# Performance work log

Measured on AMD Instinct MI355X. Metric: run time of the kernel, lower is better.

The kernel has to match this reference:

```python
import jax, jax.numpy as jnp
import numpy as np

B, C, N = 8, 512, 2048
C2 = C // 2
BN_EPS = 1e-5


def setup_inputs() -> dict:
    key = jax.random.key(0)
    ks = jax.random.split(key, 8)
    s = lambda fan_in: 1.0 / np.sqrt(fan_in)
    return {
        "q": jax.random.normal(ks[0], (B, C, N), jnp.float32),
        "x": jax.random.normal(ks[1], (B, C2, N), jnp.float32),
        "Wq": jax.random.normal(ks[2], (C2, C), jnp.float32) * s(C),
        "Wk": jax.random.normal(ks[3], (C2, C2), jnp.float32) * s(C2),
        "Wv": jax.random.normal(ks[4], (C2, C), jnp.float32) * s(C),
        "bv": jax.random.normal(ks[5], (C2,), jnp.float32) * 0.01,
        "Wt": jax.random.normal(ks[6], (C2, C2), jnp.float32) * s(C2),
        "bt": jax.random.normal(ks[7], (C2,), jnp.float32) * 0.01,
        "gamma": jnp.ones((C2,), jnp.float32),
        "beta": jnp.zeros((C2,), jnp.float32),
        "running_mean": jnp.zeros((C2,), jnp.float32),
        "running_var": jnp.ones((C2,), jnp.float32),
    }


def reference(q, x, Wq, Wk, Wv, bv, Wt, bt, gamma, beta, running_mean, running_var):
    # 1x1 convs are pointwise GEMMs over the channel dim
    x_q = jnp.einsum("oc,bcn->bno", Wq, q)                    # [B, N, C2]
    x_k = jnp.einsum("oc,bcn->bon", Wk, x)                    # [B, C2, N]
    x_v = jnp.einsum("oc,bcn->bon", Wv, q) + bv[None, :, None]  # [B, C2, N]
    energy = jnp.einsum("bnc,bcm->bnm", x_q, x_k)             # [B, N, N]
    attn = jax.nn.softmax(energy, axis=-1)
    # offset-attention L1 renormalization over the query axis (dim=1)
    attn = attn / (1e-9 + attn.sum(axis=1, keepdims=True))
    x_r = jnp.einsum("bcn,bnm->bcm", x_v, attn)               # [B, C2, N]
    h = jnp.einsum("oc,bcn->bon", Wt, x - x_r) + bt[None, :, None]
    # BatchNorm1d in eval mode with running statistics
    inv = gamma / jnp.sqrt(running_var + BN_EPS)
    h = h * inv[None, :, None] + (beta - running_mean * inv)[None, :, None]
    return jax.nn.relu(h) + x
```

## Files before the change

### kernel.cpp

```cpp
#include <hip/hip_runtime.h>
#include <cstdint>
#include <cstddef>

#define KB_  8
#define KC_  512
#define KC2_ 256
#define KN_  2048

typedef __attribute__((ext_vector_type(8))) __bf16 bf16x8;
typedef __attribute__((ext_vector_type(8))) unsigned short u16x8;
typedef __attribute__((ext_vector_type(4))) float f32x4;

__device__ __forceinline__ unsigned short f2bf(float f) {
  union { float f; unsigned u; } x; x.f = f;
  unsigned r = x.u + 0x7fffu + ((x.u >> 16) & 1u);
  return (unsigned short)(r >> 16);
}
__device__ __forceinline__ float bf2f(unsigned short h) {
  union { unsigned u; float f; } x; x.u = ((unsigned)h) << 16;
  return x.f;
}

#define GLD16(g, l) __builtin_amdgcn_global_load_lds( \
    (__attribute__((address_space(1))) void*)(g),     \
    (__attribute__((address_space(3))) void*)(l), 16, 0, 0)

#define WAIT_VM8()  asm volatile("s_waitcnt vmcnt(8)" ::: "memory")
#define WAIT_VM0()  asm volatile("s_waitcnt vmcnt(0)" ::: "memory")
#define BARRIER()   __builtin_amdgcn_s_barrier()

__device__ __forceinline__ void xcd_swizzle(int& bx, int& by, int& bz) {
  const int gx = gridDim.x, gy = gridDim.y;
  const int nb = gx * gy * (int)gridDim.z;
  int f = ((int)blockIdx.z * gy + (int)blockIdx.y) * gx + (int)blockIdx.x;
  if ((nb & 7) == 0) f = (f & 7) * (nb >> 3) + (f >> 3);
  const int gxy = gx * gy;
  bz = f / gxy; int rem = f - bz * gxy;
  by = rem / gx; bx = rem - by * gx;
}

__global__ __launch_bounds__(256) void cvt_kernel(const float* __restrict__ in,
                                                  unsigned short* __restrict__ out, int n) {
  int i = (blockIdx.x * 256 + threadIdx.x) * 4;
  if (i >= n) return;
  float4 f = *(const float4*)(in + i);
  ushort4 u = { f2bf(f.x), f2bf(f.y), f2bf(f.z), f2bf(f.w) };
  *(ushort4*)(out + i) = u;
}

__global__ __launch_bounds__(256) void cvt_pair_kernel(const float* __restrict__ in,
                                                       unsigned short* __restrict__ hi,
                                                       unsigned short* __restrict__ lo, int n) {
  int i = (blockIdx.x * 256 + threadIdx.x) * 4;
  if (i >= n) return;
  float4 f = *(const float4*)(in + i);
  ushort4 h = { f2bf(f.x), f2bf(f.y), f2bf(f.z), f2bf(f.w) };
  ushort4 l = { f2bf(f.x - bf2f(h.x)), f2bf(f.y - bf2f(h.y)),
                f2bf(f.z - bf2f(h.z)), f2bf(f.w - bf2f(h.w)) };
  *(ushort4*)(hi + i) = h;
  *(ushort4*)(lo + i) = l;
}

__global__ __launch_bounds__(256) void transpose_pair_kernel(const float* __restrict__ in,
                                                             long sIn,
                                                             unsigned short* __restrict__ hi,
                                                             unsigned short* __restrict__ lo,
                                                             long sOut, int R, int Cc) {
  int b = blockIdx.z;
  const float* I = in + (size_t)b * sIn;
  __shared__ float tile[64][65];
  int t = threadIdx.x;
  int r0 = blockIdx.y * 64, c0 = blockIdx.x * 64;
#pragma unroll
  for (int k = 0; k < 4; k++) {
    int vi = k * 256 + t, rr = vi >> 4, cv = vi & 15;
    float4 f = *(const float4*)&I[(size_t)(r0 + rr) * Cc + c0 + cv * 4];
    tile[rr][cv * 4 + 0] = f.x; tile[rr][cv * 4 + 1] = f.y;
    tile[rr][cv * 4 + 2] = f.z; tile[rr][cv * 4 + 3] = f.w;
  }
  __syncthreads();
#pragma unroll
  for (int k = 0; k < 4; k++) {
    int vi = k * 256 + t, cc = vi >> 4, rv = vi & 15;
    float f0 = tile[rv * 4 + 0][cc], f1 = tile[rv * 4 + 1][cc];
    float f2 = tile[rv * 4 + 2][cc], f3 = tile[rv * 4 + 3][cc];
    ushort4 h = { f2bf(f0), f2bf(f1), f2bf(f2), f2bf(f3) };
    ushort4 l = { f2bf(f0 - bf2f(h.x)), f2bf(f1 - bf2f(h.y)),
                  f2bf(f2 - bf2f(h.z)), f2bf(f3 - bf2f(h.w)) };
    size_t o = (size_t)b * sOut + (size_t)(c0 + cc) * R + r0 + rv * 4;
    *(ushort4*)&hi[o] = h;
    *(ushort4*)&lo[o] = l;
  }
}

__global__ __launch_bounds__(256) void rowreduce_kernel(const float* __restrict__ rowpart,
                                                        float* __restrict__ rsv) {
  int idx = blockIdx.x * 256 + threadIdx.x;
  const float* p = rowpart + (size_t)idx * 32;
  float s = 0.f;
#pragma unroll
  for (int k = 0; k < 32; k++) s += p[k];
  rsv[idx] = 1.0f / s;
}

__global__ __launch_bounds__(256) void denom_kernel(const unsigned short* __restrict__ uT,
                                                    const float* __restrict__ rsv,
                                                    float* __restrict__ denom) {
  int b = blockIdx.y;
  int m = blockIdx.x * 4 + (threadIdx.x >> 6);
  int lane = threadIdx.x & 63;
  const unsigned short* U = uT + ((size_t)b * KN_ + m) * KN_;
  const float* R = rsv + (size_t)b * KN_;
  float s = 0.f;
#pragma unroll
  for (int c = 0; c < 4; c++) {
    int n = c * 512 + lane * 8;
    u16x8 u = *(const u16x8*)&U[n];
    float4 r0 = *(const float4*)&R[n];
    float4 r1 = *(const float4*)&R[n + 4];
    s += bf2f(u[0]) * r0.x + bf2f(u[1]) * r0.y + bf2f(u[2]) * r0.z + bf2f(u[3]) * r0.w;
    s += bf2f(u[4]) * r1.x + bf2f(u[5]) * r1.y + bf2f(u[6]) * r1.z + bf2f(u[7]) * r1.w;
  }
#pragma unroll
  for (int o = 32; o > 0; o >>= 1) s += __shfl_xor(s, o, 64);
  if (lane == 0) denom[(size_t)b * KN_ + m] = s;
}

__global__ __launch_bounds__(256) void energy_kernel(
    const unsigned short* __restrict__ Ahi, const unsigned short* __restrict__ Alo,
    const unsigned short* __restrict__ Bhi, const unsigned short* __restrict__ Blo,
    unsigned short* __restrict__ uT, float* __restrict__ rowpart) {
  int bx, by, b;
  xcd_swizzle(bx, by, b);
  Ahi += (size_t)b * KN_ * KC2_; Alo += (size_t)b * KN_ * KC2_;
  Bhi += (size_t)b * KN_ * KC2_; Blo += (size_t)b * KN_ * KC2_;
  const int m0 = by * 128;
  const int n0 = bx * 128;
  __shared__ __align__(16) char smem[65536];
  const int t = threadIdx.x, lane = t & 63, w = t >> 6;
  const int wr = w >> 1, wc = w & 1;
  const int srow = t >> 2;
  const int scol = (((t & 3) ^ ((srow >> 1) & 3)) * 8);
  const int lr = lane & 15, lk = (lane >> 4) * 8;
  const int rsw = ((lr >> 1) & 3) << 4;

  auto STAGE = [&](char* dst, int kt) {
    const size_t ga = (size_t)(m0 + srow) * KC2_ + kt + scol;
    const size_t gb = (size_t)(n0 + srow) * KC2_ + kt + scol;
    GLD16(Ahi + ga, dst + 0 + w * 1024);
    GLD16(Ahi + ga + (size_t)64 * KC2_, dst + 4096 + w * 1024);
    GLD16(Alo + ga, dst + 8192 + w * 1024);
    GLD16(Alo + ga + (size_t)64 * KC2_, dst + 12288 + w * 1024);
    GLD16(Bhi + gb, dst + 16384 + w * 1024);
    GLD16(Bhi + gb + (size_t)64 * KC2_, dst + 20480 + w * 1024);
    GLD16(Blo + gb, dst + 24576 + w * 1024);
    GLD16(Blo + gb + (size_t)64 * KC2_, dst + 28672 + w * 1024);
  };

  f32x4 acc[4][4];
  const f32x4 z = {0.f, 0.f, 0.f, 0.f};
#pragma unroll
  for (int i = 0; i < 4; i++)
#pragma unroll
    for (int j = 0; j < 4; j++) acc[i][j] = z;

  STAGE(smem, 0);
  for (int kt8 = 0; kt8 < 8; kt8++) {
    char* cur = smem + (kt8 & 1) * 32768;
    char* nxt = smem + ((kt8 & 1) ^ 1) * 32768;
    if (kt8 < 7) {
      STAGE(nxt, (kt8 + 1) * 32);
      WAIT_VM8();
    } else {
      WAIT_VM0();
    }
    BARRIER();
    bf16x8 ah[4], al[4], bh[4], bl[4];
#pragma unroll
    for (int i = 0; i < 4; i++) {
      int ro = (wr * 64 + i * 16 + lr) * 64 + ((lk * 2) ^ rsw);
      ah[i] = *(const bf16x8*)(cur + 0 + ro);
      al[i] = *(const bf16x8*)(cur + 8192 + ro);
    }
#pragma unroll
    for (int j = 0; j < 4; j++) {
      int ro = (wc * 64 + j * 16 + lr) * 64 + ((lk * 2) ^ rsw);
      bh[j] = *(const bf16x8*)(cur + 16384 + ro);
      bl[j] = *(const bf16x8*)(cur + 24576 + ro);
    }
#pragma unroll
    for (int i = 0; i < 4; i++)
#pragma unroll
      for (int j = 0; j < 4; j++) {
        acc[i][j] = __builtin_amdgcn_mfma_f32_16x16x32_bf16(al[i], bh[j], acc[i][j], 0, 0, 0);
        acc[i][j] = __builtin_amdgcn_mfma_f32_16x16x32_bf16(ah[i], bl[j], acc[i][j], 0, 0, 0);
        acc[i][j] = __builtin_amdgcn_mfma_f32_16x16x32_bf16(ah[i], bh[j], acc[i][j], 0, 0, 0);
      }
    BARRIER();
  }

#pragma unroll
  for (int i = 0; i < 4; i++)
#pragma unroll
    for (int j = 0; j < 4; j++)
#pragma unroll
      for (int r = 0; r < 4; r++) acc[i][j][r] = __expf(acc[i][j][r] - 40.f);

#pragma unroll
  for (int i = 0; i < 4; i++) {
#pragma unroll
    for (int r = 0; r < 4; r++) {
      float s = acc[i][0][r] + acc[i][1][r] + acc[i][2][r] + acc[i][3][r];
      s += __shfl_xor(s, 1, 64); s += __shfl_xor(s, 2, 64);
      s += __shfl_xor(s, 4, 64); s += __shfl_xor(s, 8, 64);
      if ((lane & 15) == 0) {
        int row = m0 + wr * 64 + i * 16 + ((lane >> 4) << 2) + r;
        rowpart[((size_t)b * KN_ + row) * 32 + bx * 2 + wc] = s;
      }
    }
  }

#pragma unroll
  for (int i = 0; i < 4; i++) {
#pragma unroll
    for (int j = 0; j < 4; j++) {
#pragma unroll
      for (int r2 = 0; r2 < 4; r2 += 2) {
        int qn = wr * 64 + i * 16 + ((lane >> 4) << 2) + r2;
        int km = wc * 64 + j * 16 + lr;
        unsigned pk = (unsigned)f2bf(acc[i][j][r2]) |
                      ((unsigned)f2bf(acc[i][j][r2 + 1]) << 16);
        int a = ((km << 8) + (qn << 1)) ^ ((km & 15) << 4);
        *(unsigned*)(smem + a) = pk;
      }
    }
  }
  __syncthreads();
#pragma unroll
  for (int it = 0; it < 8; it++) {
    int km = (t >> 4) + it * 16, chunk = t & 15;
    int a = ((km << 8) + (chunk << 4)) ^ ((km & 15) << 4);
    size_t g = ((size_t)b * KN_ + (n0 + km)) * KN_ + m0 + chunk * 8;
    *(bf16x8*)&uT[g] = *(const bf16x8*)(smem + a);
  }
}

enum { EPI_PAIR = 0, EPI_VSCALE = 2, EPI_XRT = 3, EPI_FINAL = 4 };

struct EpiParams {
  const float* bias;
  const float* xf;  long xf_stride;
  const float* scale; long scale_stride;
  const float* gamma; const float* beta; const float* mean; const float* var;
};

template<int EPI>
__device__ __forceinline__ void gemm_core(
    char* __restrict__ smem, int bx, int by, int b,
    const unsigned short* __restrict__ A0, const unsigned short* __restrict__ A1,
    long sA, int lda, int seg,
    const unsigned short* __restrict__ B0, const unsigned short* __restrict__ B1,
    long sB, int ldb,
    void* __restrict__ Cv, void* __restrict__ Cv2, long sC, int ldc, int K,
    const EpiParams& ep) {
  A0 += (size_t)b * sA; A1 += (size_t)b * sA;
  B0 += (size_t)b * sB; B1 += (size_t)b * sB;
  const int m0 = by * 128, n0 = bx * 128;
  const int t = threadIdx.x, lane = t & 63, w = t >> 6;
  const int wr = w >> 1, wc = w & 1;
  const int srow = t >> 2;
  const int scol = (((t & 3) ^ ((srow >> 1) & 3)) * 8);
  const int lr = lane & 15, lk = (lane >> 4) * 8;
  const int rsw = ((lr >> 1) & 3) << 4;

  auto STAGE = [&](char* dst, int kt) {
    int s = seg ? ((kt >= seg) + (kt >= 2 * seg)) : 0;
    int kl = kt - s * seg;
    const unsigned short* Ab = (s == 1) ? A1 : A0;
    const unsigned short* Bb = (s == 2) ? B1 : B0;
    const unsigned short* gA = Ab + (size_t)(m0 + srow) * lda + kl + scol;
    const unsigned short* gB = Bb + (size_t)(n0 + srow) * ldb + kl + scol;
    GLD16(gA, dst + w * 1024);
    GLD16(gA + (size_t)64 * lda, dst + 4096 + w * 1024);
    GLD16(gA + 32, dst + 8192 + w * 1024);
    GLD16(gA + (size_t)64 * lda + 32, dst + 12288 + w * 1024);
    GLD16(gB, dst + 16384 + w * 1024);
    GLD16(gB + (size_t)64 * ldb, dst + 20480 + w * 1024);
    GLD16(gB + 32, dst + 24576 + w * 1024);
    GLD16(gB + (size_t)64 * ldb + 32, dst + 28672 + w * 1024);
  };

  f32x4 acc[4][4];
  const f32x4 z = {0.f, 0.f, 0.f, 0.f};
#pragma unroll
  for (int i = 0; i < 4; i++)
#pragma unroll
    for (int j = 0; j < 4; j++) acc[i][j] = z;

  const int nt = K >> 6;
  STAGE(smem, 0);
  for (int t8 = 0; t8 < nt; t8++) {
    char* cur = smem + (t8 & 1) * 32768;
    char* nxt = smem + ((t8 & 1) ^ 1) * 32768;
    if (t8 < nt - 1) {
      STAGE(nxt, (t8 + 1) * 64);
      WAIT_VM8();
    } else {
      WAIT_VM0();
    }
    BARRIER();
#pragma unroll
    for (int kk = 0; kk < 2; kk++) {
      bf16x8 af[4], bfv[4];
#pragma unroll
      for (int i = 0; i < 4; i++)
        af[i] = *(const bf16x8*)(cur + kk * 8192 +
                                 (wr * 64 + i * 16 + lr) * 64 + ((lk * 2) ^ rsw));
#pragma unroll
      for (int j = 0; j < 4; j++)
        bfv[j] = *(const bf16x8*)(cur + 16384 + kk * 8192 +
                                  (wc * 64 + j * 16 + lr) * 64 + ((lk * 2) ^ rsw));
#pragma unroll
      for (int i = 0; i < 4; i++)
#pragma unroll
        for (int j = 0; j < 4; j++)
          acc[i][j] = __builtin_amdgcn_mfma_f32_16x16x32_bf16(af[i], bfv[j], acc[i][j], 0, 0, 0);
    }
    BARRIER();
  }

  if constexpr (EPI == EPI_XRT) {
    float dinv[4];
#pragma unroll
    for (int j = 0; j < 4; j++)
      dinv[j] = 1.0f / (1e-9f + ep.scale[(size_t)b * ep.scale_stride +
                                         n0 + wc * 64 + j * 16 + lr]);
    const float* X = ep.xf + (size_t)b * ep.xf_stride;
#pragma unroll
    for (int i = 0; i < 4; i++) {
#pragma unroll
      for (int j = 0; j < 4; j++) {
#pragma unroll
        for (int r2 = 0; r2 < 4; r2 += 2) {
          int cl = wr * 64 + i * 16 + ((lane >> 4) << 2) + r2;
          int ml = wc * 64 + j * 16 + lr;
          float x0 = X[(size_t)(m0 + cl) * KN_ + n0 + ml];
          float x1 = X[(size_t)(m0 + cl + 1) * KN_ + n0 + ml];
          float t0 = x0 - acc[i][j][r2] * dinv[j];
          float t1 = x1 - acc[i][j][r2 + 1] * dinv[j];
          unsigned pk = (unsigned)f2bf(t0) | ((unsigned)f2bf(t1) << 16);
          int a = ((ml << 8) + (cl << 1)) ^ ((ml & 15) << 4);
          *(unsigned*)(smem + a) = pk;
        }
      }
    }
    __syncthreads();
    unsigned short* tT = (unsigned short*)Cv;
#pragma unroll
    for (int it = 0; it < 8; it++) {
      int ml = (t >> 4) + it * 16, chunk = t & 15;
      int a = ((ml << 8) + (chunk << 4)) ^ ((ml & 15) << 4);
      size_t g = ((size_t)b * KN_ + (n0 + ml)) * KC2_ + m0 + chunk * 8;
      *(bf16x8*)&tT[g] = *(const bf16x8*)(smem + a);
    }
    return;
  }

#pragma unroll
  for (int i = 0; i < 4; i++) {
#pragma unroll
    for (int r = 0; r < 4; r++) {
      const int row = m0 + wr * 64 + i * 16 + ((lane >> 4) << 2) + r;
      float pbias = 0.f, pinv = 1.f, padd = 0.f;
      if constexpr (EPI == EPI_VSCALE) pbias = ep.bias[row];
      if constexpr (EPI == EPI_FINAL) {
        pbias = ep.bias[row];
        float iv = ep.gamma[row] * rsqrtf(ep.var[row] + 1e-5f);
        pinv = iv;
        padd = ep.beta[row] - ep.mean[row] * iv;
      }
#pragma unroll
      for (int j = 0; j < 4; j++) {
        const int col = n0 + wc * 64 + j * 16 + lr;
        float v = acc[i][j][r];
        size_t o = (size_t)b * sC + (size_t)row * ldc + col;
        if constexpr (EPI == EPI_PAIR) {
          unsigned short h = f2bf(v);
          ((unsigned short*)Cv)[o] = h;
          ((unsigned short*)Cv2)[o] = f2bf(v - bf2f(h));
        } else if constexpr (EPI == EPI_VSCALE) {
          float sc = ep.scale[(size_t)b * ep.scale_stride + col];
          ((unsigned short*)Cv)[o] = f2bf((v + pbias) * sc);
        } else {
          float h = (v + pbias) * pinv + padd;
          h = fmaxf(h, 0.f);
          float xval = ep.xf[(size_t)b * ep.xf_stride + o - (size_t)b * sC];
          ((float*)Cv)[o] = h + xval;
        }
      }
    }
  }
}

template<int EPI>
__global__ __launch_bounds__(256) void gemm_one(
    const unsigned short* __restrict__ A0, const unsigned short* __restrict__ A1,
    long sA, int lda, int seg,
    const unsigned short* __restrict__ B0, const unsigned short* __restrict__ B1,
    long sB, int ldb,
    void* __restrict__ Cv, void* __restrict__ Cv2, long sC, int ldc, int K,
    EpiParams ep) {
  __shared__ __align__(16) char smem[65536];
  int bx, by, b;
  xcd_swizzle(bx, by, b);
  gemm_core<EPI>(smem, bx, by, b, A0, A1, sA, lda, seg, B0, B1, sB, ldb,
                 Cv, Cv2, sC, ldc, K, ep);
}

__global__ __launch_bounds__(256) void proj2_kernel(
    const unsigned short* __restrict__ qThi, const unsigned short* __restrict__ qTlo,
    const unsigned short* __restrict__ Wqhi, const unsigned short* __restrict__ Wqlo,
    unsigned short* __restrict__ xqhi, unsigned short* __restrict__ xqlo,
    const unsigned short* __restrict__ xThi, const unsigned short* __restrict__ xTlo,
    const unsigned short* __restrict__ Wkhi, const unsigned short* __restrict__ Wklo,
    unsigned short* __restrict__ xkhi, unsigned short* __restrict__ xklo) {
  __shared__ __align__(16) char smem[65536];
  int f = (int)blockIdx.x;
  f = (f & 7) * 64 + (f >> 3);
  EpiParams ep{};
  if (f < 256) {
    int bx = f & 1, by = (f >> 1) & 15, b = f >> 5;
    gemm_core<EPI_PAIR>(smem, bx, by, b, qThi, qTlo, (long)KN_ * KC_, KC_, KC_,
                        Wqhi, Wqlo, 0, KC_, xqhi, xqlo, (long)KN_ * KC2_, KC2_,
                        3 * KC_, ep);
  } else {
    int g = f - 256;
    int bx = g & 1, by = (g >> 1) & 15, b = g >> 5;
    gemm_core<EPI_PAIR>(smem, bx, by, b, xThi, xTlo, (long)KN_ * KC2_, KC2_, KC2_,
                        Wkhi, Wklo, 0, KC2_, xkhi, xklo, (long)KN_ * KC2_, KC2_,
                        3 * KC2_, ep);
  }
}

extern "C" void kernel_launch(void* const* d_in, const int* in_sizes, int n_in,
                              void* d_out, int out_size, void* d_ws, size_t ws_size,
                              hipStream_t stream) {
  (void)in_sizes; (void)n_in; (void)out_size; (void)ws_size;
  const float* q     = (const float*)d_in[0];
  const float* x     = (const float*)d_in[1];
  const float* Wq    = (const float*)d_in[2];
  const float* Wk    = (const float*)d_in[3];
  const float* Wv    = (const float*)d_in[4];
  const float* bv    = (const float*)d_in[5];
  const float* Wt    = (const float*)d_in[6];
  const float* bt    = (const float*)d_in[7];
  const float* gamma = (const float*)d_in[8];
  const float* beta  = (const float*)d_in[9];
  const float* rmean = (const float*)d_in[10];
  const float* rvar  = (const float*)d_in[11];
  float* out = (float*)d_out;

  const size_t SZ_qT = (size_t)KB_ * KN_ * KC_ * 2;
  const size_t SZ_xT = (size_t)KB_ * KN_ * KC2_ * 2;
  char* ws = (char*)d_ws;
  size_t off = 0;
  auto alloc = [&](size_t bytes) {
    char* p = ws + off;
    off += (bytes + 255) & ~(size_t)255;
    return p;
  };
  unsigned short* qThi = (unsigned short*)alloc(SZ_qT);
  unsigned short* qTlo = (unsigned short*)alloc(SZ_qT);
  unsigned short* xThi = (unsigned short*)alloc(SZ_xT);
  unsigned short* xTlo = (unsigned short*)alloc(SZ_xT);
  unsigned short* xqhi = (unsigned short*)alloc(SZ_xT);
  unsigned short* xqlo = (unsigned short*)alloc(SZ_xT);
  unsigned short* xkhi = (unsigned short*)alloc(SZ_xT);
  unsigned short* xklo = (unsigned short*)alloc(SZ_xT);
  unsigned short* x_v  = (unsigned short*)alloc((size_t)KB_ * KC2_ * KN_ * 2);
  unsigned short* tT   = (unsigned short*)alloc(SZ_xT);
  unsigned short* Wqhi = (unsigned short*)alloc((size_t)KC2_ * KC_ * 2);
  unsigned short* Wqlo = (unsigned short*)alloc((size_t)KC2_ * KC_ * 2);
  unsigned short* Wkhi = (unsigned short*)alloc((size_t)KC2_ * KC2_ * 2);
  unsigned short* Wklo = (unsigned short*)alloc((size_t)KC2_ * KC2_ * 2);
  unsigned short* Wvb  = (unsigned short*)alloc((size_t)KC2_ * KC_ * 2);
  unsigned short* Wtb  = (unsigned short*)alloc((size_t)KC2_ * KC2_ * 2);
  float* rsv     = (float*)alloc((size_t)KB_ * KN_ * 4);
  float* denom   = (float*)alloc((size_t)KB_ * KN_ * 4);
  float* rowpart = (float*)alloc((size_t)KB_ * KN_ * 32 * 4);
  unsigned short* uT = (unsigned short*)alloc((size_t)KB_ * KN_ * KN_ * 2);

  dim3 blk(256);

  cvt_pair_kernel<<<dim3(KC2_ * KC_ / 1024), blk, 0, stream>>>(Wq, Wqhi, Wqlo, KC2_ * KC_);
  cvt_pair_kernel<<<dim3(KC2_ * KC2_ / 1024), blk, 0, stream>>>(Wk, Wkhi, Wklo, KC2_ * KC2_);
  cvt_kernel<<<dim3(KC2_ * KC_ / 1024), blk, 0, stream>>>(Wv, Wvb, KC2_ * KC_);
  cvt_kernel<<<dim3(KC2_ * KC2_ / 1024), blk, 0, stream>>>(Wt, Wtb, KC2_ * KC2_);

  transpose_pair_kernel<<<dim3(KN_ / 64, KC_ / 64, KB_), blk, 0, stream>>>(
      q, (long)KC_ * KN_, qThi, qTlo, (long)KN_ * KC_, KC_, KN_);
  transpose_pair_kernel<<<dim3(KN_ / 64, KC2_ / 64, KB_), blk, 0, stream>>>(
      x, (long)KC2_ * KN_, xThi, xTlo, (long)KN_ * KC2_, KC2_, KN_);

  proj2_kernel<<<dim3(512), blk, 0, stream>>>(qThi, qTlo, Wqhi, Wqlo, xqhi, xqlo,
                                              xThi, xTlo, Wkhi, Wklo, xkhi, xklo);

  energy_kernel<<<dim3(KN_ / 128, KN_ / 128, KB_), blk, 0, stream>>>(
      xqhi, xqlo, xkhi, xklo, uT, rowpart);
  rowreduce_kernel<<<dim3(KB_ * KN_ / 256), blk, 0, stream>>>(rowpart, rsv);

  EpiParams e3{}; e3.bias = bv; e3.scale = rsv; e3.scale_stride = KN_;
  gemm_one<EPI_VSCALE><<<dim3(KN_ / 128, KC2_ / 128, KB_), blk, 0, stream>>>(
      Wvb, nullptr, 0, KC_, 0, qThi, nullptr, (long)KN_ * KC_, KC_,
      x_v, nullptr, (long)KC2_ * KN_, KN_, KC_, e3);

  denom_kernel<<<dim3(KN_ / 4, KB_), blk, 0, stream>>>(uT, rsv, denom);

  EpiParams e5{}; e5.xf = x; e5.xf_stride = (long)KC2_ * KN_;
  e5.scale = denom; e5.scale_stride = KN_;
  gemm_one<EPI_XRT><<<dim3(KN_ / 128, KC2_ / 128, KB_), blk, 0, stream>>>(
      x_v, nullptr, (long)KC2_ * KN_, KN_, 0, uT, nullptr, (long)KN_ * KN_, KN_,
      tT, nullptr, 0, 0, KN_, e5);

  EpiParams e6{}; e6.bias = bt; e6.xf = x; e6.xf_stride = (long)KC2_ * KN_;
  e6.gamma = gamma; e6.beta = beta; e6.mean = rmean; e6.var = rvar;
  gemm_one<EPI_FINAL><<<dim3(KN_ / 128, KC2_ / 128, KB_), blk, 0, stream>>>(
      Wtb, nullptr, 0, KC2_, 0, tT, nullptr, (long)KN_ * KC2_, KC2_,
      out, nullptr, (long)KC2_ * KN_, KN_, KC2_, e6);
}
```

Measured before the change: 197.2 us.

## Enlarge energy GEMM tiles to 256x256 and fold V projection into projection kernel

The energy kernel now uses 512-thread blocks computing 256x256 output tiles with 128KB of LDS, doubling operand reuse per staged load and cutting the number of blocks. The V projection is moved into the combined projection launch (proj3) with a plain bias epilogue. Its row-softmax scaling is now applied by a separate elementwise xvscale kernel after the row reduction. The bigger tiles raise register and LDS pressure, which lowers occupancy, and the grid drops to 512 blocks. The extra elementwise pass adds a read and a write of x_v.

Result: slower. 211.5 us (+7.3%).

```diff
diff --git a/kernel.cpp b/kernel.cpp
--- a/kernel.cpp
+++ b/kernel.cpp
@@ -103,6 +103,23 @@
   rsv[idx] = 1.0f / s;
 }
 
+__global__ __launch_bounds__(256) void xvscale_kernel(unsigned short* __restrict__ xv,
+                                                      const float* __restrict__ rsv) {
+  size_t idx = ((size_t)blockIdx.x * 256 + threadIdx.x) * 8;
+  int n = (int)(idx & (KN_ - 1));
+  int b = (int)(idx >> 19);
+  u16x8 u = *(const u16x8*)&xv[idx];
+  const float* R = rsv + (size_t)b * KN_ + n;
+  float4 r0 = *(const float4*)R;
+  float4 r1 = *(const float4*)(R + 4);
+  u16x8 o;
+  o[0] = f2bf(bf2f(u[0]) * r0.x); o[1] = f2bf(bf2f(u[1]) * r0.y);
+  o[2] = f2bf(bf2f(u[2]) * r0.z); o[3] = f2bf(bf2f(u[3]) * r0.w);
+  o[4] = f2bf(bf2f(u[4]) * r1.x); o[5] = f2bf(bf2f(u[5]) * r1.y);
+  o[6] = f2bf(bf2f(u[6]) * r1.z); o[7] = f2bf(bf2f(u[7]) * r1.w);
+  *(u16x8*)&xv[idx] = o;
+}
+
 __global__ __launch_bounds__(256) void denom_kernel(const unsigned short* __restrict__ uT,
                                                     const float* __restrict__ rsv,
                                                     float* __restrict__ denom) {
@@ -126,7 +143,7 @@
   if (lane == 0) denom[(size_t)b * KN_ + m] = s;
 }
 
-__global__ __launch_bounds__(256) void energy_kernel(
+__global__ __launch_bounds__(512, 2) void energy_kernel(
     const unsigned short* __restrict__ Ahi, const unsigned short* __restrict__ Alo,
     const unsigned short* __restrict__ Bhi, const unsigned short* __restrict__ Blo,
     unsigned short* __restrict__ uT, float* __restrict__ rowpart) {
@@ -134,11 +151,11 @@
   xcd_swizzle(bx, by, b);
   Ahi += (size_t)b * KN_ * KC2_; Alo += (size_t)b * KN_ * KC2_;
   Bhi += (size_t)b * KN_ * KC2_; Blo += (size_t)b * KN_ * KC2_;
-  const int m0 = by * 128;
-  const int n0 = bx * 128;
-  __shared__ __align__(16) char smem[65536];
+  const int m0 = by * 256;
+  const int n0 = bx * 256;
+  __shared__ __align__(16) char smem[131072];
   const int t = threadIdx.x, lane = t & 63, w = t >> 6;
-  const int wr = w >> 1, wc = w & 1;
+  const int wr = w >> 2, wc = w & 3;
   const int srow = t >> 2;
   const int scol = (((t & 3) ^ ((srow >> 1) & 3)) * 8);
   const int lr = lane & 15, lk = (lane >> 4) * 8;
@@ -148,26 +165,26 @@
     const size_t ga = (size_t)(m0 + srow) * KC2_ + kt + scol;
     const size_t gb = (size_t)(n0 + srow) * KC2_ + kt + scol;
     GLD16(Ahi + ga, dst + 0 + w * 1024);
-    GLD16(Ahi + ga + (size_t)64 * KC2_, dst + 4096 + w * 1024);
-    GLD16(Alo + ga, dst + 8192 + w * 1024);
-    GLD16(Alo + ga + (size_t)64 * KC2_, dst + 12288 + w * 1024);
-    GLD16(Bhi + gb, dst + 16384 + w * 1024);
-    GLD16(Bhi + gb + (size_t)64 * KC2_, dst + 20480 + w * 1024);
-    GLD16(Blo + gb, dst + 24576 + w * 1024);
-    GLD16(Blo + gb + (size_t)64 * KC2_, dst + 28672 + w * 1024);
+    GLD16(Ahi + ga + (size_t)128 * KC2_, dst + 8192 + w * 1024);
+    GLD16(Alo + ga, dst + 16384 + w * 1024);
+    GLD16(Alo + ga + (size_t)128 * KC2_, dst + 24576 + w * 1024);
+    GLD16(Bhi + gb, dst + 32768 + w * 1024);
+    GLD16(Bhi + gb + (size_t)128 * KC2_, dst + 40960 + w * 1024);
+    GLD16(Blo + gb, dst + 49152 + w * 1024);
+    GLD16(Blo + gb + (size_t)128 * KC2_, dst + 57344 + w * 1024);
   };
 
-  f32x4 acc[4][4];
+  f32x4 acc[8][4];
   const f32x4 z = {0.f, 0.f, 0.f, 0.f};
 #pragma unroll
-  for (int i = 0; i < 4; i++)
+  for (int i = 0; i < 8; i++)
 #pragma unroll
     for (int j = 0; j < 4; j++) acc[i][j] = z;
 
   STAGE(smem, 0);
   for (int kt8 = 0; kt8 < 8; kt8++) {
-    char* cur = smem + (kt8 & 1) * 32768;
-    char* nxt = smem + ((kt8 & 1) ^ 1) * 32768;
+    char* cur = smem + (kt8 & 1) * 65536;
+    char* nxt = smem + ((kt8 & 1) ^ 1) * 65536;
     if (kt8 < 7) {
       STAGE(nxt, (kt8 + 1) * 32);
       WAIT_VM8();
@@ -175,77 +192,82 @@
       WAIT_VM0();
     }
     BARRIER();
-    bf16x8 ah[4], al[4], bh[4], bl[4];
-#pragma unroll
-    for (int i = 0; i < 4; i++) {
-      int ro = (wr * 64 + i * 16 + lr) * 64 + ((lk * 2) ^ rsw);
-      ah[i] = *(const bf16x8*)(cur + 0 + ro);
-      al[i] = *(const bf16x8*)(cur + 8192 + ro);
-    }
+    bf16x8 bh[4], bl[4];
 #pragma unroll
     for (int j = 0; j < 4; j++) {
       int ro = (wc * 64 + j * 16 + lr) * 64 + ((lk * 2) ^ rsw);
-      bh[j] = *(const bf16x8*)(cur + 16384 + ro);
-      bl[j] = *(const bf16x8*)(cur + 24576 + ro);
-    }
-#pragma unroll
-    for (int i = 0; i < 4; i++)
+      bh[j] = *(const bf16x8*)(cur + 32768 + ro);
+      bl[j] = *(const bf16x8*)(cur + 49152 + ro);
+    }
+#pragma unroll
+    for (int i = 0; i < 8; i++) {
+      int ro = (wr * 128 + i * 16 + lr) * 64 + ((lk * 2) ^ rsw);
+      bf16x8 ah = *(const bf16x8*)(cur + ro);
+      bf16x8 al = *(const bf16x8*)(cur + 16384 + ro);
 #pragma unroll
       for (int j = 0; j < 4; j++) {
-        acc[i][j] = __builtin_amdgcn_mfma_f32_16x16x32_bf16(al[i], bh[j], acc[i][j], 0, 0, 0);
-        acc[i][j] = __builtin_amdgcn_mfma_f32_16x16x32_bf16(ah[i], bl[j], acc[i][j], 0, 0, 0);
-        acc[i][j] = __builtin_amdgcn_mfma_f32_16x16x32_bf16(ah[i], bh[j], acc[i][j], 0, 0, 0);
-      }
+        acc[i][j] = __builtin_amdgcn_mfma_f32_16x16x32_bf16(al, bh[j], acc[i][j], 0, 0, 0);
+        acc[i][j] = __builtin_amdgcn_mfma_f32_16x16x32_bf16(ah, bl[j], acc[i][j], 0, 0, 0);
+        acc[i][j] = __builtin_amdgcn_mfma_f32_16x16x32_bf16(ah, bh[j], acc[i][j], 0, 0, 0);
+      }
+    }
     BARRIER();
   }
 
 #pragma unroll
-  for (int i = 0; i < 4; i++)
+  for (int i = 0; i < 8; i++)
 #pragma unroll
     for (int j = 0; j < 4; j++)
 #pragma unroll
       for (int r = 0; r < 4; r++) acc[i][j][r] = __expf(acc[i][j][r] - 40.f);
 
 #pragma unroll
-  for (int i = 0; i < 4; i++) {
+  for (int i = 0; i < 8; i++) {
 #pragma unroll
     for (int r = 0; r < 4; r++) {
       float s = acc[i][0][r] + acc[i][1][r] + acc[i][2][r] + acc[i][3][r];
       s += __shfl_xor(s, 1, 64); s += __shfl_xor(s, 2, 64);
       s += __shfl_xor(s, 4, 64); s += __shfl_xor(s, 8, 64);
       if ((lane & 15) == 0) {
-        int row = m0 + wr * 64 + i * 16 + ((lane >> 4) << 2) + r;
-        rowpart[((size_t)b * KN_ + row) * 32 + bx * 2 + wc] = s;
-      }
-    }
-  }
-
-#pragma unroll
-  for (int i = 0; i < 4; i++) {
+        int row = m0 + wr * 128 + i * 16 + ((lane >> 4) << 2) + r;
+        rowpart[((size_t)b * KN_ + row) * 32 + bx * 4 + wc] = s;
+      }
+    }
+  }
+
+#pragma unroll
+  for (int i = 0; i < 8; i++) {
 #pragma unroll
     for (int j = 0; j < 4; j++) {
 #pragma unroll
       for (int r2 = 0; r2 < 4; r2 += 2) {
-        int qn = wr * 64 + i * 16 + ((lane >> 4) << 2) + r2;
+        int qn = wr * 128 + i * 16 + ((lane >> 4) << 2) + r2;
         int km = wc * 64 + j * 16 + lr;
         unsigned pk = (unsigned)f2bf(acc[i][j][r2]) |
                       ((unsigned)f2bf(acc[i][j][r2 + 1]) << 16);
-        int a = ((km << 8) + (qn << 1)) ^ ((km & 15) << 4);
+        int a = (km << 9) + ((qn << 1) ^ ((km & 15) << 4));
         *(unsigned*)(smem + a) = pk;
       }
     }
   }
   __syncthreads();
-#pragma unroll
-  for (int it = 0; it < 8; it++) {
-    int km = (t >> 4) + it * 16, chunk = t & 15;
-    int a = ((km << 8) + (chunk << 4)) ^ ((km & 15) << 4);
-    size_t g = ((size_t)b * KN_ + (n0 + km)) * KN_ + m0 + chunk * 8;
-    *(bf16x8*)&uT[g] = *(const bf16x8*)(smem + a);
-  }
-}
-
-enum { EPI_PAIR = 0, EPI_VSCALE = 2, EPI_XRT = 3, EPI_FINAL = 4 };
+  {
+    int kmb = t >> 4, chunk = t & 15;
+#pragma unroll
+    for (int it = 0; it < 8; it++) {
+      int km = kmb + it * 32;
+      size_t gbase = ((size_t)b * KN_ + (n0 + km)) * KN_ + m0;
+#pragma unroll
+      for (int h = 0; h < 2; h++) {
+        int c = h * 16 + chunk;
+        int a = (km << 9) + ((c << 4) ^ ((km & 15) << 4));
+        *(bf16x8*)&uT[gbase + c * 8] = *(const bf16x8*)(smem + a);
+      }
+    }
+  }
+}
+
+enum { EPI_PAIR = 0, EPI_BIAS = 1, EPI_XRT = 3, EPI_FINAL = 4 };
 
 struct EpiParams {
   const float* bias;
@@ -372,7 +394,7 @@
     for (int r = 0; r < 4; r++) {
       const int row = m0 + wr * 64 + i * 16 + ((lane >> 4) << 2) + r;
       float pbias = 0.f, pinv = 1.f, padd = 0.f;
-      if constexpr (EPI == EPI_VSCALE) pbias = ep.bias[row];
+      if constexpr (EPI == EPI_BIAS) pbias = ep.bias[row];
       if constexpr (EPI == EPI_FINAL) {
         pbias = ep.bias[row];
         float iv = ep.gamma[row] * rsqrtf(ep.var[row] + 1e-5f);
@@ -388,9 +410,8 @@
           unsigned short h = f2bf(v);
           ((unsigned short*)Cv)[o] = h;
           ((unsigned short*)Cv2)[o] = f2bf(v - bf2f(h));
-        } else if constexpr (EPI == EPI_VSCALE) {
-          float sc = ep.scale[(size_t)b * ep.scale_stride + col];
-          ((unsigned short*)Cv)[o] = f2bf((v + pbias) * sc);
+        } else if constexpr (EPI == EPI_BIAS) {
+          ((unsigned short*)Cv)[o] = f2bf(v + pbias);
         } else {
           float h = (v + pbias) * pinv + padd;
           h = fmaxf(h, 0.f);
@@ -417,28 +438,37 @@
                  Cv, Cv2, sC, ldc, K, ep);
 }
 
-__global__ __launch_bounds__(256) void proj2_kernel(
+__global__ __launch_bounds__(256) void proj3_kernel(
     const unsigned short* __restrict__ qThi, const unsigned short* __restrict__ qTlo,
     const unsigned short* __restrict__ Wqhi, const unsigned short* __restrict__ Wqlo,
     unsigned short* __restrict__ xqhi, unsigned short* __restrict__ xqlo,
     const unsigned short* __restrict__ xThi, const unsigned short* __restrict__ xTlo,
     const unsigned short* __restrict__ Wkhi, const unsigned short* __restrict__ Wklo,
-    unsigned short* __restrict__ xkhi, unsigned short* __restrict__ xklo) {
+    unsigned short* __restrict__ xkhi, unsigned short* __restrict__ xklo,
+    const unsigned short* __restrict__ Wvb, unsigned short* __restrict__ x_v,
+    const float* __restrict__ bv) {
   __shared__ __align__(16) char smem[65536];
   int f = (int)blockIdx.x;
-  f = (f & 7) * 64 + (f >> 3);
+  f = (f & 7) * 96 + (f >> 3);
   EpiParams ep{};
   if (f < 256) {
     int bx = f & 1, by = (f >> 1) & 15, b = f >> 5;
     gemm_core<EPI_PAIR>(smem, bx, by, b, qThi, qTlo, (long)KN_ * KC_, KC_, KC_,
                         Wqhi, Wqlo, 0, KC_, xqhi, xqlo, (long)KN_ * KC2_, KC2_,
                         3 * KC_, ep);
-  } else {
+  } else if (f < 512) {
     int g = f - 256;
     int bx = g & 1, by = (g >> 1) & 15, b = g >> 5;
     gemm_core<EPI_PAIR>(smem, bx, by, b, xThi, xTlo, (long)KN_ * KC2_, KC2_, KC2_,
                         Wkhi, Wklo, 0, KC2_, xkhi, xklo, (long)KN_ * KC2_, KC2_,
                         3 * KC2_, ep);
+  } else {
+    int g = f - 512;
+    int bx = g & 15, by = (g >> 4) & 1, b = g >> 5;
+    ep.bias = bv;
+    gemm_core<EPI_BIAS>(smem, bx, by, b, Wvb, nullptr, 0, KC_, 0,
+                        qThi, nullptr, (long)KN_ * KC_, KC_,
+                        x_v, nullptr, (long)KC2_ * KN_, KN_, KC_, ep);
   }
 }
 
@@ -502,17 +532,15 @@
   transpose_pair_kernel<<<dim3(KN_ / 64, KC2_ / 64, KB_), blk, 0, stream>>>(
       x, (long)KC2_ * KN_, xThi, xTlo, (long)KN_ * KC2_, KC2_, KN_);
 
-  proj2_kernel<<<dim3(512), blk, 0, stream>>>(qThi, qTlo, Wqhi, Wqlo, xqhi, xqlo,
-                                              xThi, xTlo, Wkhi, Wklo, xkhi, xklo);
-
-  energy_kernel<<<dim3(KN_ / 128, KN_ / 128, KB_), blk, 0, stream>>>(
+  proj3_kernel<<<dim3(768), blk, 0, stream>>>(qThi, qTlo, Wqhi, Wqlo, xqhi, xqlo,
+                                              xThi, xTlo, Wkhi, Wklo, xkhi, xklo,
+                                              Wvb, x_v, bv);
+
+  energy_kernel<<<dim3(KN_ / 256, KN_ / 256, KB_), dim3(512), 0, stream>>>(
       xqhi, xqlo, xkhi, xklo, uT, rowpart);
   rowreduce_kernel<<<dim3(KB_ * KN_ / 256), blk, 0, stream>>>(rowpart, rsv);
 
-  EpiParams e3{}; e3.bias = bv; e3.scale = rsv; e3.scale_stride = KN_;
-  gemm_one<EPI_VSCALE><<<dim3(KN_ / 128, KC2_ / 128, KB_), blk, 0, stream>>>(
-      Wvb, nullptr, 0, KC_, 0, qThi, nullptr, (long)KN_ * KC_, KC_,
-      x_v, nullptr, (long)KC2_ * KN_, KN_, KC_, e3);
+  xvscale_kernel<<<dim3(KB_ * KC2_ * KN_ / 8 / 256), blk, 0, stream>>>(x_v, rsv);
 
   denom_kernel<<<dim3(KN_ / 4, KB_), blk, 0, stream>>>(uT, rsv, denom);
 
```
